# Kernel tuning notes

Hardware: AMD Instinct MI355X
Metric: run time of the kernel (lower is better)

Reference implementation:

```python
import jax, jax.numpy as jnp
import numpy as np

K_GRAD = 20        # num_nbrs for gradient operator
K_NORMAL = 10      # knn for normal/basis estimation
GRAD_REG = 1e-3    # grad_reg (lambda)
KERNEL_WIDTH = 1.0 # grad_kernel_width
EPS = 1e-8
N1, N2 = 8192, 8192
CHANNELS = [3, 64, 128, 256]


def knn_idx(pos, k):
    # brute-force kNN incl. self (loop=True, target_to_source)
    sq = jnp.sum(pos * pos, axis=1)
    d2 = sq[:, None] + sq[None, :] - 2.0 * (pos @ pos.T)
    _, idx = jax.lax.top_k(-d2, k)
    return idx  # [N, k]


def estimate_basis(pos, nbr, orientation):
    rel = pos[nbr] - pos[:, None, :]              # [N,k,3]
    cov = jnp.einsum('nki,nkj->nij', rel, rel)    # [N,3,3] local PCA
    _, vecs = jnp.linalg.eigh(cov)                # ascending eigenvalues
    normal, x_basis = vecs[:, :, 0], vecs[:, :, 2]
    sign = jnp.where(jnp.sum(normal * orientation, -1, keepdims=True) < 0.0, -1.0, 1.0)
    normal = normal * sign                        # orient along `orientation`
    y_basis = jnp.cross(normal, x_basis)
    return normal, x_basis, y_basis


def build_grad_div(pos, x_basis, y_basis, nbr):
    # regularized, Gaussian-weighted least-squares fit of a linear function per neighborhood
    rel = pos[nbr] - pos[:, None, :]              # [N,k,3]
    u = jnp.einsum('nkd,nd->nk', rel, x_basis)    # tangent coords
    v = jnp.einsum('nkd,nd->nk', rel, y_basis)
    dist = jnp.sqrt(jnp.sum(rel * rel, -1) + EPS)
    h = jnp.mean(dist, axis=1, keepdims=True)     # per-point bandwidth
    w = jnp.exp(-(dist * dist) / ((KERNEL_WIDTH * h) ** 2 + EPS))
    B = jnp.stack([jnp.ones_like(u), u, v], -1)   # [N,k,3] design matrix
    BtW = jnp.swapaxes(B, 1, 2) * w[:, None, :]   # [N,3,k]
    A = BtW @ B + GRAD_REG * jnp.eye(3, dtype=pos.dtype)
    C = jnp.linalg.solve(A, BtW)                  # [N,3,k] LS coefficients
    Gx, Gy = C[:, 1, :], C[:, 2, :]               # gradient stencils
    basis = jnp.stack([x_basis, y_basis], -1)     # [N,3,2]
    R = jnp.einsum('nda,nkdb->nkab', basis, basis[nbr])  # transport j->i, [N,k,2,2]
    return Gx, Gy, R


def grad_apply(Gx, Gy, nbr, f):
    fn = f[nbr]                                   # [N,k,C]
    return jnp.stack([jnp.einsum('nk,nkc->nc', Gx, fn),
                      jnp.einsum('nk,nkc->nc', Gy, fn)], 1)  # [N,2,C]


def div_apply(Gx, Gy, R, nbr, v):
    vt = jnp.einsum('nkab,nkbc->nkac', R, v[nbr])  # transported neighbor vectors
    return (jnp.einsum('nk,nkc->nc', Gx, vt[:, :, 0]) +
            jnp.einsum('nk,nkc->nc', Gy, vt[:, :, 1]))


def delta_conv(x, v, nbr, Gx, Gy, R, Ws, bs, Wv, bv, centralized):
    xn = x[nbr]
    if centralized:
        xn = xn - x[:, None, :]
    xmax = jnp.max(xn, axis=1)                    # max aggregation
    dv = div_apply(Gx, Gy, R, nbr, v)             # divergence
    Jv = jnp.stack([-v[:, 1], v[:, 0]], 1)        # 90-degree rotation
    cv = div_apply(Gx, Gy, R, nbr, Jv)            # curl = div(J v)
    x_out = jax.nn.relu(jnp.concatenate([xmax, dv, cv], -1) @ Ws + bs)
    if Wv is None:
        return x_out, v                            # last layer: scalar only
    gv = grad_apply(Gx, Gy, nbr, x_out)           # [N,2,Cout]
    vo = jnp.concatenate([v, gv], -1) @ Wv        # channel mix, no bias (equivariant)
    n = jnp.sqrt(jnp.sum(vo * vo, axis=1, keepdims=True) + EPS)
    vo = vo * (jax.nn.relu(n + bv) / (n + EPS))   # norm-gated vector nonlinearity
    return x_out, vo


def _forward(points, als_ppoints, params):
    pos = jnp.concatenate([points, als_ppoints], axis=0)  # [N,3]
    nbr = knn_idx(pos, K_GRAD)
    nbr_n = knn_idx(pos, K_NORMAL)
    _, xb, yb = estimate_basis(pos, nbr_n, orientation=pos)
    Gx, Gy, R = build_grad_div(pos, xb, yb, nbr)
    x = pos
    v = grad_apply(Gx, Gy, nbr, x)                # v = grad @ x
    out = []
    for i, (Ws, bs, Wv, bv) in enumerate(params):
        x, v = delta_conv(x, v, nbr, Gx, Gy, R, Ws, bs, Wv, bv, centralized=(i == 0))
        out.append(x)
    return tuple(out)


def setup_inputs():
    key = jax.random.key(0)
    ks = jax.random.split(key, 8)
    inp = {
        'points': jax.random.normal(ks[0], (N1, 3), jnp.float32),
        'als_ppoints': jax.random.normal(ks[1], (N2, 3), jnp.float32),
    }
    ki = 2
    for i in range(3):
        cin, cout = CHANNELS[i], CHANNELS[i + 1]
        inp[f'Ws{i}'] = jax.random.normal(ks[ki], (3 * cin, cout), jnp.float32) / np.sqrt(3.0 * cin)
        inp[f'bs{i}'] = jnp.zeros((cout,), jnp.float32)
        ki += 1
        if i < 2:
            inp[f'Wv{i}'] = jax.random.normal(ks[ki], (cin + cout, cout), jnp.float32) / np.sqrt(float(cin + cout))
            inp[f'bv{i}'] = jnp.zeros((cout,), jnp.float32)
            ki += 1
    return inp


def reference(points, als_ppoints, Ws0, bs0, Wv0, bv0, Ws1, bs1, Wv1, bv1, Ws2, bs2):
    params = [(Ws0, bs0, Wv0, bv0), (Ws1, bs1, Wv1, bv1), (Ws2, bs2, None, None)]
    return _forward(points, als_ppoints, params)
```

## Files before the change

### kernel.cpp

```cpp
#include <hip/hip_runtime.h>
#include <math.h>

#define NPTS 16384
#define KG 20
#define KN 10
#define KC 8
#define EPSF 1e-8f

#define GDIM 32
#define GL 4.75f
#define CW 0.296875f
#define GINV 3.3684210526f
#define RMAX 6

typedef __attribute__((ext_vector_type(8))) short short8v;
typedef __attribute__((ext_vector_type(4))) float floatx4;

__device__ __forceinline__ unsigned short f2bf(float v) {
  union { float f; unsigned u; } x;
  x.f = v;
  unsigned r = x.u + 0x7FFFu + ((x.u >> 16) & 1u);
  return (unsigned short)(r >> 16);
}

__device__ __forceinline__ float bf2f(unsigned short u) {
  union { unsigned u32; float f; } x;
  x.u32 = (unsigned)u << 16;
  return x.f;
}

#define KNN_INSERT(d2v, iv)                                                 \
  if ((d2v) < dist[KG - 1]) {                                               \
    dist[KG - 1] = (d2v); idx[KG - 1] = (iv);                               \
    _Pragma("unroll")                                                       \
    for (int s_ = KG - 1; s_ > 0; --s_) {                                   \
      if (dist[s_] < dist[s_ - 1]) {                                        \
        float td_ = dist[s_]; dist[s_] = dist[s_ - 1]; dist[s_ - 1] = td_;  \
        int ti_ = idx[s_]; idx[s_] = idx[s_ - 1]; idx[s_ - 1] = ti_;        \
      }                                                                     \
    }                                                                       \
  }

#define KNN_INSERT8(d2v, iv)                                                \
  if ((d2v) < dist[KC - 1]) {                                               \
    dist[KC - 1] = (d2v); idx[KC - 1] = (iv);                               \
    _Pragma("unroll")                                                       \
    for (int s_ = KC - 1; s_ > 0; --s_) {                                   \
      if (dist[s_] < dist[s_ - 1]) {                                        \
        float td_ = dist[s_]; dist[s_] = dist[s_ - 1]; dist[s_ - 1] = td_;  \
        int ti_ = idx[s_]; idx[s_] = idx[s_ - 1]; idx[s_ - 1] = ti_;        \
      }                                                                     \
    }                                                                       \
  }

__global__ __launch_bounds__(256) void posbin_kernel(const float* __restrict__ pts,
                                                     const float* __restrict__ als,
                                                     float4* __restrict__ pos4,
                                                     int* __restrict__ cell_count,
                                                     int* __restrict__ pt_cell) {
  int n = blockIdx.x * 256 + threadIdx.x;
  if (n >= NPTS) return;
  const float* src = (n < 8192) ? (pts + (size_t)n * 3) : (als + (size_t)(n - 8192) * 3);
  float x = src[0], y = src[1], z = src[2];
  pos4[n] = make_float4(x, y, z, 0.f);
  int cxi = (int)floorf((x + GL) * GINV); cxi = min(max(cxi, 0), GDIM - 1);
  int cyi = (int)floorf((y + GL) * GINV); cyi = min(max(cyi, 0), GDIM - 1);
  int czi = (int)floorf((z + GL) * GINV); czi = min(max(czi, 0), GDIM - 1);
  int c = (czi * GDIM + cyi) * GDIM + cxi;
  pt_cell[n] = c;
  atomicAdd(&cell_count[c], 1);
}

__global__ __launch_bounds__(256) void zero_kernel(int* __restrict__ cell_count,
                                                   int* __restrict__ fb_count) {
  int i = blockIdx.x * 256 + threadIdx.x;
  if (i < GDIM * GDIM * GDIM) cell_count[i] = 0;
  if (i == 0) *fb_count = 0;
}

__device__ __forceinline__ int cell_of(float x) {
  int c = (int)floorf((x + GL) * GINV);
  return min(max(c, 0), GDIM - 1);
}

__global__ __launch_bounds__(1024) void scan_kernel(const int* __restrict__ cell_count,
                                                    int* __restrict__ cell_start,
                                                    int* __restrict__ cell_cursor) {
  __shared__ int s[1024];
  int tid = threadIdx.x;
  int base = tid * 32;
  int local[32];
  int sum = 0;
#pragma unroll
  for (int i = 0; i < 32; ++i) { local[i] = cell_count[base + i]; sum += local[i]; }
  s[tid] = sum;
  __syncthreads();
  for (int off = 1; off < 1024; off <<= 1) {
    int v = (tid >= off) ? s[tid - off] : 0;
    __syncthreads();
    s[tid] += v;
    __syncthreads();
  }
  int run = s[tid] - sum;
#pragma unroll
  for (int i = 0; i < 32; ++i) {
    cell_start[base + i] = run;
    cell_cursor[base + i] = run;
    run += local[i];
  }
}

__global__ __launch_bounds__(256) void scatter_kernel(const float4* __restrict__ pos4,
                                                      const int* __restrict__ pt_cell,
                                                      int* __restrict__ cell_cursor,
                                                      float4* __restrict__ sorted4) {
  int i = blockIdx.x * 256 + threadIdx.x;
  if (i >= NPTS) return;
  int c = pt_cell[i];
  int dst = atomicAdd(&cell_cursor[c], 1);
  float4 p = pos4[i];
  p.w = __int_as_float(i);
  sorted4[dst] = p;
}

__global__ __launch_bounds__(256) void knn_grid_kernel(const float4* __restrict__ sorted4,
                                                       const int* __restrict__ cell_start,
                                                       const int* __restrict__ cell_count,
                                                       int* __restrict__ nbr,
                                                       int* __restrict__ fb_list,
                                                       int* __restrict__ fb_count) {
  int lane = threadIdx.x & 63;
  int sub = lane >> 5;
  int sl = lane & 31;
  int qs = blockIdx.x * 8 + (threadIdx.x >> 6) * 2 + sub;
  if (qs >= NPTS) return;
  float4 p = sorted4[qs];
  int q = __float_as_int(p.w);
  int cx = cell_of(p.x), cy = cell_of(p.y), cz = cell_of(p.z);
  float dist[KC];
  int idx[KC];
#pragma unroll
  for (int i = 0; i < KC; ++i) { dist[i] = 3.4e38f; idx[i] = 0; }

  {
    int tot = 0;
    int x0 = max(cx - 1, 0), x1 = min(cx + 1, GDIM - 1);
    int zlo = max(cz - 1, 0), zhi = min(cz + 1, GDIM - 1);
    int ylo = max(cy - 1, 0), yhi = min(cy + 1, GDIM - 1);
    for (int z = zlo; z <= zhi; ++z) {
      for (int y = ylo; y <= yhi; ++y) {
        int c0 = (z * GDIM + y) * GDIM + x0;
        int c1 = (z * GDIM + y) * GDIM + x1;
        int beg = cell_start[c0];
        int end = cell_start[c1] + cell_count[c1];
        int off = (sl - tot) & 31;
        for (int j = beg + off; j < end; j += 32) {
          float4 sp = sorted4[j];
          float dx = sp.x - p.x, dy = sp.y - p.y, dz = sp.z - p.z;
          float d2 = dx * dx + dy * dy + dz * dz;
          KNN_INSERT8(d2, __float_as_int(sp.w));
        }
        tot += end - beg;
      }
    }
  }
  int done;
  {
    float b2 = CW * CW;
    int cnt = 0;
#pragma unroll
    for (int i = 0; i < KC; ++i) cnt += (dist[i] <= b2) ? 1 : 0;
#pragma unroll
    for (int s = 1; s < 32; s <<= 1) cnt += __shfl_xor(cnt, s, 64);
    done = (cnt >= KG) ? 1 : 0;
  }

  for (int r = 2; r <= RMAX && !done; ++r) {
    int side = 2 * r + 1;
    int nt = side * side;
    for (int t = sl; t < nt; t += 32) {
      int dz = t / side - r;
      int dy = t - (dz + r) * side - r;
      int z = cz + dz, y = cy + dy;
      if (z < 0 || z >= GDIM || y < 0 || y >= GDIM) continue;
      int rowbase = (z * GDIM + y) * GDIM;
      if (dz == -r || dz == r || dy == -r || dy == r) {
        int xa = max(cx - r, 0), xb = min(cx + r, GDIM - 1);
        int beg = cell_start[rowbase + xa];
        int end = cell_start[rowbase + xb] + cell_count[rowbase + xb];
        for (int j = beg; j < end; ++j) {
          float4 sp = sorted4[j];
          float ddx = sp.x - p.x, ddy = sp.y - p.y, ddz = sp.z - p.z;
          float d2 = ddx * ddx + ddy * ddy + ddz * ddz;
          KNN_INSERT8(d2, __float_as_int(sp.w));
        }
      } else {
        int x = cx - r;
        if (x >= 0) {
          int c = rowbase + x;
          int beg = cell_start[c], end = beg + cell_count[c];
          for (int j = beg; j < end; ++j) {
            float4 sp = sorted4[j];
            float ddx = sp.x - p.x, ddy = sp.y - p.y, ddz = sp.z - p.z;
            float d2 = ddx * ddx + ddy * ddy + ddz * ddz;
            KNN_INSERT8(d2, __float_as_int(sp.w));
          }
        }
        x = cx + r;
        if (x < GDIM) {
          int c = rowbase + x;
          int beg = cell_start[c], end = beg + cell_count[c];
          for (int j = beg; j < end; ++j) {
            float4 sp = sorted4[j];
            float ddx = sp.x - p.x, ddy = sp.y - p.y, ddz = sp.z - p.z;
            float d2 = ddx * ddx + ddy * ddy + ddz * ddz;
            KNN_INSERT8(d2, __float_as_int(sp.w));
          }
        }
      }
    }
    float b = CW * (float)r;
    float b2 = b * b;
    int cnt = 0;
#pragma unroll
    for (int i = 0; i < KC; ++i) cnt += (dist[i] <= b2) ? 1 : 0;
#pragma unroll
    for (int s = 1; s < 32; s <<= 1) cnt += __shfl_xor(cnt, s, 64);
    if (cnt >= KG) done = 1;
  }

  int popc = 0, ovf = 0;
  for (int round = 0; round < KG; ++round) {
    unsigned long long key = ((unsigned long long)__float_as_uint(dist[0]) << 14) |
                             (unsigned long long)(unsigned)idx[0];
    unsigned long long m = key;
#pragma unroll
    for (int s = 1; s < 32; s <<= 1) {
      unsigned long long o = __shfl_xor(m, s, 64);
      if (o < m) m = o;
    }
    if (key == m) {
      nbr[(size_t)q * KG + round] = (int)(m & 0x3FFF);
#pragma unroll
      for (int s = 0; s < KC - 1; ++s) { dist[s] = dist[s + 1]; idx[s] = idx[s + 1]; }
      dist[KC - 1] = 3.4e38f;
      idx[KC - 1] = 0;
      if (++popc == KC) ovf = 1;
    }
  }
#pragma unroll
  for (int s = 1; s < 32; s <<= 1) ovf |= __shfl_xor(ovf, s, 64);
  if ((ovf || !done) && sl == 0) {
    int s = atomicAdd(fb_count, 1);
    fb_list[s] = qs;
  }
}

__global__ __launch_bounds__(256) void knn_fb_kernel(const float4* __restrict__ sorted4,
                                                     const int* __restrict__ fb_list,
                                                     const int* __restrict__ fb_count,
                                                     int* __restrict__ nbr) {
  __shared__ unsigned long long lists[256 * KG];
  __shared__ unsigned long long heads[256];
  __shared__ unsigned long long winner;
  int tid = threadIdx.x;
  int cnt = *fb_count;
  for (int qi = blockIdx.x; qi < cnt; qi += gridDim.x) {
    int t = fb_list[qi];
    float4 p = sorted4[t];
    int q = __float_as_int(p.w);
    float dist[KG];
    int idx[KG];
#pragma unroll
    for (int i = 0; i < KG; ++i) { dist[i] = 3.4e38f; idx[i] = 0; }
    int j0 = tid * 64;
    for (int j = j0; j < j0 + 64; ++j) {
      float4 c = sorted4[j];
      float dx = c.x - p.x, dy = c.y - p.y, dz = c.z - p.z;
      float d2 = dx * dx + dy * dy + dz * dz;
      KNN_INSERT(d2, __float_as_int(c.w));
    }
#pragma unroll
    for (int i = 0; i < KG; ++i)
      lists[tid * KG + i] = ((unsigned long long)__float_as_uint(dist[i]) << 22) |
                            ((unsigned long long)(unsigned)idx[i] << 8) |
                            (unsigned long long)tid;
    int hp = 0;
    __syncthreads();
    for (int round = 0; round < KG; ++round) {
      heads[tid] = (hp < KG) ? lists[tid * KG + hp] : ~0ull;
      __syncthreads();
      if (tid < 64) {
        unsigned long long m = heads[tid];
        unsigned long long o = heads[tid + 64];  if (o < m) m = o;
        o = heads[tid + 128]; if (o < m) m = o;
        o = heads[tid + 192]; if (o < m) m = o;
#pragma unroll
        for (int s = 32; s > 0; s >>= 1) {
          unsigned long long x = __shfl_xor(m, s, 64);
          if (x < m) m = x;
        }
        if (tid == 0) winner = m;
      }
      __syncthreads();
      unsigned long long w = winner;
      if (tid == (int)(w & 0xFF)) hp++;
      if (tid == 0) nbr[(size_t)q * KG + round] = (int)((w >> 8) & 0x3FFF);
      __syncthreads();
    }
  }
}

__global__ __launch_bounds__(256) void basis_kernel(const float4* __restrict__ pos4,
                                                    const int* __restrict__ nbr,
                                                    float4* __restrict__ xb4,
                                                    float4* __restrict__ yb4) {
  int n = blockIdx.x * 256 + threadIdx.x;
  if (n >= NPTS) return;
  float4 p = pos4[n];
  double c00 = 0, c01 = 0, c02 = 0, c11 = 0, c12 = 0, c22 = 0;
  for (int k = 0; k < KN; ++k) {
    int m = nbr[(size_t)n * KG + k];
    float4 pm = pos4[m];
    double dx = (double)pm.x - p.x, dy = (double)pm.y - p.y, dz = (double)pm.z - p.z;
    c00 += dx * dx; c01 += dx * dy; c02 += dx * dz;
    c11 += dy * dy; c12 += dy * dz; c22 += dz * dz;
  }
  double nx = 0, ny = 0, nz = 1;
  double p1 = c01 * c01 + c02 * c02 + c12 * c12;
  double qm = (c00 + c11 + c22) / 3.0;
  double g0 = c00 - qm, g1 = c11 - qm, g2 = c22 - qm;
  double p2 = g0 * g0 + g1 * g1 + g2 * g2 + 2.0 * p1;
  if (p2 > 1e-26) {
    double pp = sqrt(p2 / 6.0);
    double inv = 1.0 / pp;
    double b00 = g0 * inv, b11 = g1 * inv, b22 = g2 * inv;
    double b01 = c01 * inv, b02 = c02 * inv, b12 = c12 * inv;
    double detB = b00 * (b11 * b22 - b12 * b12) - b01 * (b01 * b22 - b12 * b02) +
                  b02 * (b01 * b12 - b11 * b02);
    double r = 0.5 * detB;
    r = fmin(1.0, fmax(-1.0, r));
    double phi = acos(r) / 3.0;
    double e1 = qm + 2.0 * pp * cos(phi);
    double e3 = qm + 2.0 * pp * cos(phi + 2.0943951023931953);
    double e2 = 3.0 * qm - e1 - e3;
    double a00 = c00 - e1, a11 = c11 - e1, a22 = c22 - e1;
    double f00 = c00 - e2, f11 = c11 - e2, f22 = c22 - e2;
    double u0 = a00 * f00 + c01 * c01 + c02 * c02;
    double u1 = c01 * f00 + a11 * c01 + c12 * c02;
    double u2 = c02 * f00 + c12 * c01 + a22 * c02;
    double v0 = a00 * c01 + c01 * f11 + c02 * c12;
    double v1 = c01 * c01 + a11 * f11 + c12 * c12;
    double v2 = c02 * c01 + c12 * f11 + a22 * c12;
    double w0 = a00 * c02 + c01 * c12 + c02 * f22;
    double w1 = c01 * c02 + a11 * c12 + c12 * f22;
    double w2 = c02 * c02 + c12 * c12 + a22 * f22;
    double nu = u0 * u0 + u1 * u1 + u2 * u2;
    double nv = v0 * v0 + v1 * v1 + v2 * v2;
    double nw = w0 * w0 + w1 * w1 + w2 * w2;
    double bx = u0, by = u1, bz = u2, bn = nu;
    if (nv > bn) { bx = v0; by = v1; bz = v2; bn = nv; }
    if (nw > bn) { bx = w0; by = w1; bz = w2; bn = nw; }
    if (bn > 1e-40) {
      double s = 1.0 / sqrt(bn);
      nx = bx * s; ny = by * s; nz = bz * s;
    }
  }
  double dotp = nx * p.x + ny * p.y + nz * p.z;
  if (dotp < 0.0) { nx = -nx; ny = -ny; nz = -nz; }
  double ax = fabs(nx), ay = fabs(ny), az = fabs(nz);
  double ex = 0, ey = 0, ez = 0;
  if (ax <= ay && ax <= az) ex = 1;
  else if (ay <= az) ey = 1;
  else ez = 1;
  double tx = ny * ez - nz * ey, ty = nz * ex - nx * ez, tz = nx * ey - ny * ex;
  double tn = 1.0 / sqrt(tx * tx + ty * ty + tz * tz);
  tx *= tn; ty *= tn; tz *= tn;
  double ux = ny * tz - nz * ty, uy = nz * tx - nx * tz, uz = nx * ty - ny * tx;
  xb4[n] = make_float4((float)tx, (float)ty, (float)tz, 0.f);
  yb4[n] = make_float4((float)ux, (float)uy, (float)uz, 0.f);
}

__global__ __launch_bounds__(256) void graddiv_kernel(const float4* __restrict__ pos4,
                                                      const int* __restrict__ nbr,
                                                      const float4* __restrict__ xb4,
                                                      const float4* __restrict__ yb4,
                                                      float* __restrict__ Gx,
                                                      float* __restrict__ Gy,
                                                      float2* __restrict__ C2,
                                                      float* __restrict__ v0) {
  int n = blockIdx.x * 256 + threadIdx.x;
  if (n >= NPTS) return;
  float4 p = pos4[n], xb = xb4[n], yb = yb4[n];
  float u[KG], vv[KG], w[KG];
  int mm[KG];
  float hsum = 0.f;
#pragma unroll
  for (int k = 0; k < KG; ++k) {
    int m = nbr[(size_t)n * KG + k];
    mm[k] = m;
    float4 pm = pos4[m];
    float rx = pm.x - p.x, ry = pm.y - p.y, rz = pm.z - p.z;
    u[k] = rx * xb.x + ry * xb.y + rz * xb.z;
    vv[k] = rx * yb.x + ry * yb.y + rz * yb.z;
    float dd = sqrtf(rx * rx + ry * ry + rz * rz + EPSF);
    w[k] = dd; hsum += dd;
  }
  float h = hsum * (1.f / KG);
  float invden = 1.f / (h * h + EPSF);
  double A00 = 0, A01 = 0, A02 = 0, A11 = 0, A12 = 0, A22 = 0;
#pragma unroll
  for (int k = 0; k < KG; ++k) {
    float wk = expf(-(w[k] * w[k]) * invden);
    w[k] = wk;
    A00 += wk; A01 += (double)wk * u[k]; A02 += (double)wk * vv[k];
    A11 += (double)wk * u[k] * u[k]; A12 += (double)wk * u[k] * vv[k];
    A22 += (double)wk * vv[k] * vv[k];
  }
  A00 += 0.001; A11 += 0.001; A22 += 0.001;
  double det = A00 * (A11 * A22 - A12 * A12) - A01 * (A01 * A22 - A12 * A02) +
               A02 * (A01 * A12 - A11 * A02);
  double idet = 1.0 / det;
  float i10 = (float)((A02 * A12 - A01 * A22) * idet);
  float i11 = (float)((A00 * A22 - A02 * A02) * idet);
  float i12 = (float)((A01 * A02 - A00 * A12) * idet);
  float i20 = (float)((A01 * A12 - A02 * A11) * idet);
  float i21 = i12;
  float i22 = (float)((A00 * A11 - A01 * A01) * idet);
  float a0x = 0, a0y = 0, a0z = 0, a1x = 0, a1y = 0, a1z = 0;
#pragma unroll
  for (int k = 0; k < KG; ++k) {
    float gx = w[k] * (i10 + i11 * u[k] + i12 * vv[k]);
    float gy = w[k] * (i20 + i21 * u[k] + i22 * vv[k]);
    Gx[(size_t)n * KG + k] = gx;
    Gy[(size_t)n * KG + k] = gy;
    int m = mm[k];
    float4 pm = pos4[m];
    a0x += gx * pm.x; a0y += gx * pm.y; a0z += gx * pm.z;
    a1x += gy * pm.x; a1y += gy * pm.y; a1z += gy * pm.z;
    float4 xm = xb4[m], ym = yb4[m];
    float g3x = gx * xb.x + gy * yb.x;
    float g3y = gx * xb.y + gy * yb.y;
    float g3z = gx * xb.z + gy * yb.z;
    float ca = g3x * xm.x + g3y * xm.y + g3z * xm.z;
    float cb = g3x * ym.x + g3y * ym.y + g3z * ym.z;
    C2[(size_t)n * KG + k] = make_float2(ca, cb);
  }
  v0[((size_t)n * 2 + 0) * 3 + 0] = a0x;
  v0[((size_t)n * 2 + 0) * 3 + 1] = a0y;
  v0[((size_t)n * 2 + 0) * 3 + 2] = a0z;
  v0[((size_t)n * 2 + 1) * 3 + 0] = a1x;
  v0[((size_t)n * 2 + 1) * 3 + 1] = a1y;
  v0[((size_t)n * 2 + 1) * 3 + 2] = a1z;
}

template <int CENTRAL>
__global__ __launch_bounds__(256) void feat16_kernel(const float* __restrict__ x, int ldx,
                                                     int cin,
                                                     const float* __restrict__ v,
                                                     const int* __restrict__ nbr,
                                                     const float2* __restrict__ C2,
                                                     unsigned short* __restrict__ feat, int Kp) {
  int per = Kp - 2 * cin;
  int gid = blockIdx.x * 256 + threadIdx.x;
  if (gid >= NPTS * per) return;
  int n = gid / per;
  int c = gid - n * per;
  size_t fb = (size_t)n * Kp;
  if (c >= cin) {
    feat[fb + 3 * cin + (c - cin)] = 0;
    return;
  }
  float xc = x[(size_t)n * ldx + c];
  float xmax = -3.4e38f, dv = 0.f, cv = 0.f;
  for (int k = 0; k < KG; ++k) {
    int m = nbr[(size_t)n * KG + k];
    float2 cc = C2[(size_t)n * KG + k];
    float xm = x[(size_t)m * ldx + c];
    xmax = fmaxf(xmax, CENTRAL ? (xm - xc) : xm);
    float va = v[((size_t)m * 2 + 0) * cin + c];
    float vb = v[((size_t)m * 2 + 1) * cin + c];
    dv += cc.x * va + cc.y * vb;
    cv += cc.y * va - cc.x * vb;
  }
  feat[fb + c] = f2bf(xmax);
  feat[fb + cin + c] = f2bf(dv);
  feat[fb + 2 * cin + c] = f2bf(cv);
}

__global__ __launch_bounds__(256) void feat16v8_kernel(const unsigned short* __restrict__ x,
                                                       int cin,
                                                       const unsigned short* __restrict__ v,
                                                       const int* __restrict__ nbr,
                                                       const float2* __restrict__ C2,
                                                       unsigned short* __restrict__ feat) {
  int per = cin >> 3;
  int gid = blockIdx.x * 256 + threadIdx.x;
  if (gid >= NPTS * per) return;
  int n = gid / per;
  int c8 = (gid - n * per) << 3;
  float xmax[8], dv[8], cv[8];
#pragma unroll
  for (int i = 0; i < 8; ++i) { xmax[i] = -3.4e38f; dv[i] = 0.f; cv[i] = 0.f; }
  const int* nrow = nbr + (size_t)n * KG;
  const float2* crow = C2 + (size_t)n * KG;
#pragma unroll 4
  for (int k = 0; k < KG; ++k) {
    int m = nrow[k];
    float2 cc = crow[k];
    short8v xm = *reinterpret_cast<const short8v*>(x + (size_t)m * cin + c8);
    short8v va = *reinterpret_cast<const short8v*>(v + ((size_t)m * 2 + 0) * cin + c8);
    short8v vb = *reinterpret_cast<const short8v*>(v + ((size_t)m * 2 + 1) * cin + c8);
#pragma unroll
    for (int i = 0; i < 8; ++i) {
      float xf = bf2f((unsigned short)xm[i]);
      float af = bf2f((unsigned short)va[i]);
      float bf = bf2f((unsigned short)vb[i]);
      xmax[i] = fmaxf(xmax[i], xf);
      dv[i] += cc.x * af + cc.y * bf;
      cv[i] += cc.y * af - cc.x * bf;
    }
  }
  size_t fb = (size_t)n * (3 * cin);
  short8v o0, o1, o2;
#pragma unroll
  for (int i = 0; i < 8; ++i) {
    o0[i] = (short)f2bf(xmax[i]);
    o1[i] = (short)f2bf(dv[i]);
    o2[i] = (short)f2bf(cv[i]);
  }
  *reinterpret_cast<short8v*>(&feat[fb + c8]) = o0;
  *reinterpret_cast<short8v*>(&feat[fb + cin + c8]) = o1;
  *reinterpret_cast<short8v*>(&feat[fb + 2 * cin + c8]) = o2;
}

__global__ __launch_bounds__(256) void vin16_kernel(const float* __restrict__ v, int cin,
                                                    const unsigned short* __restrict__ xout,
                                                    int cout,
                                                    const int* __restrict__ nbr,
                                                    const float* __restrict__ Gx,
                                                    const float* __restrict__ Gy,
                                                    unsigned short* __restrict__ vinb, int Kp,
                                                    int total) {
  int gid = blockIdx.x * 256 + threadIdx.x;
  if (gid >= total) return;
  int n = gid / Kp;
  int c = gid - n * Kp;
  int K = cin + cout;
  unsigned short o0, o1;
  if (c < cin) {
    o0 = f2bf(v[((size_t)n * 2 + 0) * cin + c]);
    o1 = f2bf(v[((size_t)n * 2 + 1) * cin + c]);
  } else if (c < K) {
    int cc = c - cin;
    float a0 = 0.f, a1 = 0.f;
    for (int k = 0; k < KG; ++k) {
      int m = nbr[(size_t)n * KG + k];
      float f = bf2f(xout[(size_t)m * cout + cc]);
      a0 += Gx[(size_t)n * KG + k] * f;
      a1 += Gy[(size_t)n * KG + k] * f;
    }
    o0 = f2bf(a0);
    o1 = f2bf(a1);
  } else {
    o0 = 0; o1 = 0;
  }
  vinb[((size_t)n * 2 + 0) * Kp + c] = o0;
  vinb[((size_t)n * 2 + 1) * Kp + c] = o1;
}

__global__ __launch_bounds__(256) void vin16v8_kernel(const unsigned short* __restrict__ v,
                                                      int cin,
                                                      const unsigned short* __restrict__ xout,
                                                      int cout,
                                                      const int* __restrict__ nbr,
                                                      const float* __restrict__ Gx,
                                                      const float* __restrict__ Gy,
                                                      unsigned short* __restrict__ vinb,
                                                      int Kp) {
  int per = Kp >> 3;
  int gid = blockIdx.x * 256 + threadIdx.x;
  if (gid >= NPTS * per) return;
  int n = gid / per;
  int c8 = (gid - n * per) << 3;
  short8v o0, o1;
  if (c8 < cin) {
    o0 = *reinterpret_cast<const short8v*>(v + ((size_t)n * 2 + 0) * cin + c8);
    o1 = *reinterpret_cast<const short8v*>(v + ((size_t)n * 2 + 1) * cin + c8);
  } else {
    int cc8 = c8 - cin;
    float a0[8], a1[8];
#pragma unroll
    for (int i = 0; i < 8; ++i) { a0[i] = 0.f; a1[i] = 0.f; }
    const int* nrow = nbr + (size_t)n * KG;
    const float* gxr = Gx + (size_t)n * KG;
    const float* gyr = Gy + (size_t)n * KG;
#pragma unroll 4
    for (int k = 0; k < KG; ++k) {
      int m = nrow[k];
      float gx = gxr[k], gy = gyr[k];
      short8v f = *reinterpret_cast<const short8v*>(xout + (size_t)m * cout + cc8);
#pragma unroll
      for (int i = 0; i < 8; ++i) {
        float ff = bf2f((unsigned short)f[i]);
        a0[i] += gx * ff;
        a1[i] += gy * ff;
      }
    }
#pragma unroll
    for (int i = 0; i < 8; ++i) {
      o0[i] = (short)f2bf(a0[i]);
      o1[i] = (short)f2bf(a1[i]);
    }
  }
  *reinterpret_cast<short8v*>(&vinb[((size_t)n * 2 + 0) * Kp + c8]) = o0;
  *reinterpret_cast<short8v*>(&vinb[((size_t)n * 2 + 1) * Kp + c8]) = o1;
}

__device__ __forceinline__ void wprep_one(const float* W, unsigned short* Wt, int K, int Kp,
                                          int N, int i) {
  int n = i / Kp, k = i - n * Kp;
  Wt[i] = (k < K) ? f2bf(W[(size_t)k * N + n]) : (unsigned short)0;
}

__global__ __launch_bounds__(256) void wprep_all_kernel(const float* __restrict__ Ws0,
                                                        const float* __restrict__ Wv0,
                                                        const float* __restrict__ Ws1,
                                                        const float* __restrict__ Wv1,
                                                        const float* __restrict__ Ws2,
                                                        unsigned short* __restrict__ Wt_s0,
                                                        unsigned short* __restrict__ Wt_v0,
                                                        unsigned short* __restrict__ Wt_s1,
                                                        unsigned short* __restrict__ Wt_v1,
                                                        unsigned short* __restrict__ Wt_s2) {
  int gid = blockIdx.x * 256 + threadIdx.x;
  if (gid < 2048) wprep_one(Ws0, Wt_s0, 9, 32, 64, gid);
  else if (gid < 8192) wprep_one(Wv0, Wt_v0, 67, 96, 64, gid - 2048);
  else if (gid < 32768) wprep_one(Ws1, Wt_s1, 192, 192, 128, gid - 8192);
  else if (gid < 57344) wprep_one(Wv1, Wt_v1, 192, 192, 128, gid - 32768);
  else if (gid < 155648) wprep_one(Ws2, Wt_s2, 384, 384, 256, gid - 57344);
}

template <int MODE>
__global__ __launch_bounds__(256) void gemm16_kernel(const unsigned short* __restrict__ A,
                                                     const unsigned short* __restrict__ Bt,
                                                     const float* __restrict__ bias,
                                                     float* __restrict__ Cf,
                                                     unsigned short* __restrict__ Cb,
                                                     int Kp, int Ncol) {
  int lane = threadIdx.x & 63;
  int wave = threadIdx.x >> 6;
  int rowBase = blockIdx.y * 64 + wave * 16;
  int colBase = blockIdx.x * 64;
  int lr = lane & 15;
  int kg = (lane >> 4) * 8;
  floatx4 acc0 = {0.f, 0.f, 0.f, 0.f};
  floatx4 acc1 = acc0, acc2 = acc0, acc3 = acc0;
  const unsigned short* arow = A + (size_t)(rowBase + lr) * Kp + kg;
  const unsigned short* b0p = Bt + (size_t)(colBase + lr) * Kp + kg;
  for (int k0 = 0; k0 < Kp; k0 += 32) {
    short8v a = *reinterpret_cast<const short8v*>(arow + k0);
    short8v b0 = *reinterpret_cast<const short8v*>(b0p + k0);
    short8v b1 = *reinterpret_cast<const short8v*>(b0p + (size_t)16 * Kp + k0);
    short8v b2 = *reinterpret_cast<const short8v*>(b0p + (size_t)32 * Kp + k0);
    short8v b3 = *reinterpret_cast<const short8v*>(b0p + (size_t)48 * Kp + k0);
    acc0 = __builtin_amdgcn_mfma_f32_16x16x32_bf16(a, b0, acc0, 0, 0, 0);
    acc1 = __builtin_amdgcn_mfma_f32_16x16x32_bf16(a, b1, acc1, 0, 0, 0);
    acc2 = __builtin_amdgcn_mfma_f32_16x16x32_bf16(a, b2, acc2, 0, 0, 0);
    acc3 = __builtin_amdgcn_mfma_f32_16x16x32_bf16(a, b3, acc3, 0, 0, 0);
  }
  int rsub = (lane >> 4) * 4;
  floatx4 accs[4] = {acc0, acc1, acc2, acc3};
#pragma unroll
  for (int nb = 0; nb < 4; ++nb) {
    int col = colBase + nb * 16 + lr;
    float bb = bias[col];
    if (MODE == 0) {
#pragma unroll
      for (int r = 0; r < 4; ++r) {
        int row = rowBase + rsub + r;
        float val = fmaxf(accs[nb][r] + bb, 0.f);
        Cf[(size_t)row * Ncol + col] = val;
        if (Cb) Cb[(size_t)row * Ncol + col] = f2bf(val);
      }
    } else {
#pragma unroll
      for (int pr = 0; pr < 2; ++pr) {
        float a0 = accs[nb][2 * pr], a1 = accs[nb][2 * pr + 1];
        float nrm = sqrtf(a0 * a0 + a1 * a1 + EPSF);
        float s = fmaxf(nrm + bb, 0.f) / (nrm + EPSF);
        int row = rowBase + rsub + 2 * pr;
        Cb[(size_t)row * Ncol + col] = f2bf(a0 * s);
        Cb[(size_t)(row + 1) * Ncol + col] = f2bf(a1 * s);
      }
    }
  }
}

extern "C" void kernel_launch(void* const* d_in, const int* in_sizes, int n_in,
                              void* d_out, int out_size, void* d_ws, size_t ws_size,
                              hipStream_t stream) {
  const float* pts = (const float*)d_in[0];
  const float* als = (const float*)d_in[1];
  const float* Ws0 = (const float*)d_in[2];
  const float* bs0 = (const float*)d_in[3];
  const float* Wv0 = (const float*)d_in[4];
  const float* bv0 = (const float*)d_in[5];
  const float* Ws1 = (const float*)d_in[6];
  const float* bs1 = (const float*)d_in[7];
  const float* Wv1 = (const float*)d_in[8];
  const float* bv1 = (const float*)d_in[9];
  const float* Ws2 = (const float*)d_in[10];
  const float* bs2 = (const float*)d_in[11];

  char* ws = (char*)d_ws;
  float4* pos4 = (float4*)(ws + 0);
  int* nbr = (int*)(ws + 262144);
  float4* xb4 = (float4*)(ws + 1572864);
  float4* yb4 = (float4*)(ws + 1835008);
  float* Gx = (float*)(ws + 2097152);
  float* Gy = (float*)(ws + 3407872);
  float2* C2 = (float2*)(ws + 4718592);
  float* v0f = (float*)(ws + 7340032);
  unsigned short* vb_a = (unsigned short*)(ws + 8388608);
  unsigned short* vb_b = (unsigned short*)(ws + 17825792);
  unsigned short* xb0m = (unsigned short*)(ws + 23068672);
  unsigned short* xb1m = (unsigned short*)(ws + 26214400);
  unsigned short* stg = (unsigned short*)(ws + 31457280);
  char* wtb = ws + 45088768;
  unsigned short* Wt_s0 = (unsigned short*)(wtb + 0);
  unsigned short* Wt_v0 = (unsigned short*)(wtb + 4096);
  unsigned short* Wt_s1 = (unsigned short*)(wtb + 16384);
  unsigned short* Wt_v1 = (unsigned short*)(wtb + 65536);
  unsigned short* Wt_s2 = (unsigned short*)(wtb + 114688);

  char* gws = ws + 46137344;
  int* cell_count = (int*)(gws + 0);
  int* cell_start = (int*)(gws + 131072);
  int* cell_cursor = (int*)(gws + 262144);
  int* pt_cell = (int*)(gws + 393216);
  int* fb_list = (int*)(gws + 458752);
  int* fb_count = (int*)(gws + 524288);
  float4* sorted4 = (float4*)(gws + 528384);

  float* out0 = (float*)d_out;
  float* out1 = out0 + (size_t)NPTS * 64;
  float* out2 = out1 + (size_t)NPTS * 128;

  zero_kernel<<<(GDIM * GDIM * GDIM + 255) / 256, 256, 0, stream>>>(cell_count, fb_count);
  posbin_kernel<<<64, 256, 0, stream>>>(pts, als, pos4, cell_count, pt_cell);
  scan_kernel<<<1, 1024, 0, stream>>>(cell_count, cell_start, cell_cursor);
  scatter_kernel<<<64, 256, 0, stream>>>(pos4, pt_cell, cell_cursor, sorted4);
  knn_grid_kernel<<<NPTS / 8, 256, 0, stream>>>(sorted4, cell_start, cell_count, nbr, fb_list,
                                                fb_count);
  knn_fb_kernel<<<128, 256, 0, stream>>>(sorted4, fb_list, fb_count, nbr);

  basis_kernel<<<64, 256, 0, stream>>>(pos4, nbr, xb4, yb4);
  graddiv_kernel<<<64, 256, 0, stream>>>(pos4, nbr, xb4, yb4, Gx, Gy, C2, v0f);

  wprep_all_kernel<<<608, 256, 0, stream>>>(Ws0, Wv0, Ws1, Wv1, Ws2, Wt_s0, Wt_v0, Wt_s1,
                                            Wt_v1, Wt_s2);

  feat16_kernel<1><<<(NPTS * 26 + 255) / 256, 256, 0, stream>>>((const float*)pos4, 4, 3, v0f,
                                                                nbr, C2, stg, 32);
  gemm16_kernel<0><<<dim3(1, 256), 256, 0, stream>>>(stg, Wt_s0, bs0, out0, xb0m, 32, 64);
  vin16_kernel<<<(NPTS * 96 + 255) / 256, 256, 0, stream>>>(v0f, 3, xb0m, 64, nbr, Gx, Gy, stg,
                                                            96, NPTS * 96);
  gemm16_kernel<1><<<dim3(1, 512), 256, 0, stream>>>(stg, Wt_v0, bv0, nullptr, vb_b, 96, 64);

  feat16v8_kernel<<<NPTS * 8 / 256, 256, 0, stream>>>(xb0m, 64, vb_b, nbr, C2, stg);
  gemm16_kernel<0><<<dim3(2, 256), 256, 0, stream>>>(stg, Wt_s1, bs1, out1, xb1m, 192, 128);
  vin16v8_kernel<<<NPTS * 24 / 256, 256, 0, stream>>>(vb_b, 64, xb1m, 128, nbr, Gx, Gy, stg,
                                                      192);
  gemm16_kernel<1><<<dim3(2, 512), 256, 0, stream>>>(stg, Wt_v1, bv1, nullptr, vb_a, 192, 128);

  feat16v8_kernel<<<NPTS * 16 / 256, 256, 0, stream>>>(xb1m, 128, vb_a, nbr, C2, stg);
  gemm16_kernel<0><<<dim3(4, 256), 256, 0, stream>>>(stg, Wt_s2, bs2, out2, nullptr, 384, 256);
}
```

Measured before the change: 322.1 us.

## Run whole pipeline in spatially sorted point order, unpermute only final outputs

Points are now indexed by their grid-sorted position throughout kNN, basis, grad/div and feature gathers, and a sortmap permutes rows back to original order only when the float outputs are written. Neighbour gathers then hit spatially local memory, which should improve cache hit rates in the gather-heavy feature and stencil kernels. The cost is an extra map array plus scattered row writes in the GEMM epilogue.

```diff
diff --git a/kernel.cpp b/kernel.cpp
--- a/kernel.cpp
+++ b/kernel.cpp
@@ -113,7 +113,8 @@
 __global__ __launch_bounds__(256) void scatter_kernel(const float4* __restrict__ pos4,
                                                       const int* __restrict__ pt_cell,
                                                       int* __restrict__ cell_cursor,
-                                                      float4* __restrict__ sorted4) {
+                                                      float4* __restrict__ sorted4,
+                                                      int* __restrict__ sortmap) {
   int i = blockIdx.x * 256 + threadIdx.x;
   if (i >= NPTS) return;
   int c = pt_cell[i];
@@ -121,6 +122,7 @@
   float4 p = pos4[i];
   p.w = __int_as_float(i);
   sorted4[dst] = p;
+  sortmap[dst] = i;
 }
 
 __global__ __launch_bounds__(256) void knn_grid_kernel(const float4* __restrict__ sorted4,
@@ -135,7 +137,6 @@
   int qs = blockIdx.x * 8 + (threadIdx.x >> 6) * 2 + sub;
   if (qs >= NPTS) return;
   float4 p = sorted4[qs];
-  int q = __float_as_int(p.w);
   int cx = cell_of(p.x), cy = cell_of(p.y), cz = cell_of(p.z);
   float dist[KC];
   int idx[KC];
@@ -158,7 +159,7 @@
           float4 sp = sorted4[j];
           float dx = sp.x - p.x, dy = sp.y - p.y, dz = sp.z - p.z;
           float d2 = dx * dx + dy * dy + dz * dz;
-          KNN_INSERT8(d2, __float_as_int(sp.w));
+          KNN_INSERT8(d2, j);
         }
         tot += end - beg;
       }
@@ -192,7 +193,7 @@
           float4 sp = sorted4[j];
           float ddx = sp.x - p.x, ddy = sp.y - p.y, ddz = sp.z - p.z;
           float d2 = ddx * ddx + ddy * ddy + ddz * ddz;
-          KNN_INSERT8(d2, __float_as_int(sp.w));
+          KNN_INSERT8(d2, j);
         }
       } else {
         int x = cx - r;
@@ -203,7 +204,7 @@
             float4 sp = sorted4[j];
             float ddx = sp.x - p.x, ddy = sp.y - p.y, ddz = sp.z - p.z;
             float d2 = ddx * ddx + ddy * ddy + ddz * ddz;
-            KNN_INSERT8(d2, __float_as_int(sp.w));
+            KNN_INSERT8(d2, j);
           }
         }
         x = cx + r;
@@ -214,7 +215,7 @@
             float4 sp = sorted4[j];
             float ddx = sp.x - p.x, ddy = sp.y - p.y, ddz = sp.z - p.z;
             float d2 = ddx * ddx + ddy * ddy + ddz * ddz;
-            KNN_INSERT8(d2, __float_as_int(sp.w));
+            KNN_INSERT8(d2, j);
           }
         }
       }
@@ -240,7 +241,7 @@
       if (o < m) m = o;
     }
     if (key == m) {
-      nbr[(size_t)q * KG + round] = (int)(m & 0x3FFF);
+      nbr[(size_t)qs * KG + round] = (int)(m & 0x3FFF);
 #pragma unroll
       for (int s = 0; s < KC - 1; ++s) { dist[s] = dist[s + 1]; idx[s] = idx[s + 1]; }
       dist[KC - 1] = 3.4e38f;
@@ -268,7 +269,6 @@
   for (int qi = blockIdx.x; qi < cnt; qi += gridDim.x) {
     int t = fb_list[qi];
     float4 p = sorted4[t];
-    int q = __float_as_int(p.w);
     float dist[KG];
     int idx[KG];
 #pragma unroll
@@ -278,7 +278,7 @@
       float4 c = sorted4[j];
       float dx = c.x - p.x, dy = c.y - p.y, dz = c.z - p.z;
       float d2 = dx * dx + dy * dy + dz * dz;
-      KNN_INSERT(d2, __float_as_int(c.w));
+      KNN_INSERT(d2, j);
     }
 #pragma unroll
     for (int i = 0; i < KG; ++i)
@@ -305,23 +305,23 @@
       __syncthreads();
       unsigned long long w = winner;
       if (tid == (int)(w & 0xFF)) hp++;
-      if (tid == 0) nbr[(size_t)q * KG + round] = (int)((w >> 8) & 0x3FFF);
+      if (tid == 0) nbr[(size_t)t * KG + round] = (int)((w >> 8) & 0x3FFF);
       __syncthreads();
     }
   }
 }
 
-__global__ __launch_bounds__(256) void basis_kernel(const float4* __restrict__ pos4,
+__global__ __launch_bounds__(256) void basis_kernel(const float4* __restrict__ sorted4,
                                                     const int* __restrict__ nbr,
                                                     float4* __restrict__ xb4,
                                                     float4* __restrict__ yb4) {
   int n = blockIdx.x * 256 + threadIdx.x;
   if (n >= NPTS) return;
-  float4 p = pos4[n];
+  float4 p = sorted4[n];
   double c00 = 0, c01 = 0, c02 = 0, c11 = 0, c12 = 0, c22 = 0;
   for (int k = 0; k < KN; ++k) {
     int m = nbr[(size_t)n * KG + k];
-    float4 pm = pos4[m];
+    float4 pm = sorted4[m];
     double dx = (double)pm.x - p.x, dy = (double)pm.y - p.y, dz = (double)pm.z - p.z;
     c00 += dx * dx; c01 += dx * dy; c02 += dx * dz;
     c11 += dy * dy; c12 += dy * dz; c22 += dz * dz;
@@ -381,7 +381,7 @@
   yb4[n] = make_float4((float)ux, (float)uy, (float)uz, 0.f);
 }
 
-__global__ __launch_bounds__(256) void graddiv_kernel(const float4* __restrict__ pos4,
+__global__ __launch_bounds__(256) void graddiv_kernel(const float4* __restrict__ sorted4,
                                                       const int* __restrict__ nbr,
                                                       const float4* __restrict__ xb4,
                                                       const float4* __restrict__ yb4,
@@ -391,7 +391,7 @@
                                                       float* __restrict__ v0) {
   int n = blockIdx.x * 256 + threadIdx.x;
   if (n >= NPTS) return;
-  float4 p = pos4[n], xb = xb4[n], yb = yb4[n];
+  float4 p = sorted4[n], xb = xb4[n], yb = yb4[n];
   float u[KG], vv[KG], w[KG];
   int mm[KG];
   float hsum = 0.f;
@@ -399,7 +399,7 @@
   for (int k = 0; k < KG; ++k) {
     int m = nbr[(size_t)n * KG + k];
     mm[k] = m;
-    float4 pm = pos4[m];
+    float4 pm = sorted4[m];
     float rx = pm.x - p.x, ry = pm.y - p.y, rz = pm.z - p.z;
     u[k] = rx * xb.x + ry * xb.y + rz * xb.z;
     vv[k] = rx * yb.x + ry * yb.y + rz * yb.z;
@@ -435,7 +435,7 @@
     Gx[(size_t)n * KG + k] = gx;
     Gy[(size_t)n * KG + k] = gy;
     int m = mm[k];
-    float4 pm = pos4[m];
+    float4 pm = sorted4[m];
     a0x += gx * pm.x; a0y += gx * pm.y; a0z += gx * pm.z;
     a1x += gy * pm.x; a1y += gy * pm.y; a1z += gy * pm.z;
     float4 xm = xb4[m], ym = yb4[m];
@@ -647,6 +647,7 @@
                                                      const float* __restrict__ bias,
                                                      float* __restrict__ Cf,
                                                      unsigned short* __restrict__ Cb,
+                                                     const int* __restrict__ rowmap,
                                                      int Kp, int Ncol) {
   int lane = threadIdx.x & 63;
   int wave = threadIdx.x >> 6;
@@ -671,6 +672,11 @@
   }
   int rsub = (lane >> 4) * 4;
   floatx4 accs[4] = {acc0, acc1, acc2, acc3};
+  int orow[4];
+  if (MODE == 0) {
+#pragma unroll
+    for (int r = 0; r < 4; ++r) orow[r] = rowmap[rowBase + rsub + r];
+  }
 #pragma unroll
   for (int nb = 0; nb < 4; ++nb) {
     int col = colBase + nb * 16 + lr;
@@ -680,7 +686,7 @@
       for (int r = 0; r < 4; ++r) {
         int row = rowBase + rsub + r;
         float val = fmaxf(accs[nb][r] + bb, 0.f);
-        Cf[(size_t)row * Ncol + col] = val;
+        Cf[(size_t)orow[r] * Ncol + col] = val;
         if (Cb) Cb[(size_t)row * Ncol + col] = f2bf(val);
       }
     } else {
@@ -742,6 +748,7 @@
   int* fb_list = (int*)(gws + 458752);
   int* fb_count = (int*)(gws + 524288);
   float4* sorted4 = (float4*)(gws + 528384);
+  int* sortmap = (int*)(gws + 790528);
 
   float* out0 = (float*)d_out;
   float* out1 = out0 + (size_t)NPTS * 64;
@@ -750,30 +757,35 @@
   zero_kernel<<<(GDIM * GDIM * GDIM + 255) / 256, 256, 0, stream>>>(cell_count, fb_count);
   posbin_kernel<<<64, 256, 0, stream>>>(pts, als, pos4, cell_count, pt_cell);
   scan_kernel<<<1, 1024, 0, stream>>>(cell_count, cell_start, cell_cursor);
-  scatter_kernel<<<64, 256, 0, stream>>>(pos4, pt_cell, cell_cursor, sorted4);
+  scatter_kernel<<<64, 256, 0, stream>>>(pos4, pt_cell, cell_cursor, sorted4, sortmap);
   knn_grid_kernel<<<NPTS / 8, 256, 0, stream>>>(sorted4, cell_start, cell_count, nbr, fb_list,
                                                 fb_count);
   knn_fb_kernel<<<128, 256, 0, stream>>>(sorted4, fb_list, fb_count, nbr);
 
-  basis_kernel<<<64, 256, 0, stream>>>(pos4, nbr, xb4, yb4);
-  graddiv_kernel<<<64, 256, 0, stream>>>(pos4, nbr, xb4, yb4, Gx, Gy, C2, v0f);
+  basis_kernel<<<64, 256, 0, stream>>>(sorted4, nbr, xb4, yb4);
+  graddiv_kernel<<<64, 256, 0, stream>>>(sorted4, nbr, xb4, yb4, Gx, Gy, C2, v0f);
 
   wprep_all_kernel<<<608, 256, 0, stream>>>(Ws0, Wv0, Ws1, Wv1, Ws2, Wt_s0, Wt_v0, Wt_s1,
                                             Wt_v1, Wt_s2);
 
-  feat16_kernel<1><<<(NPTS * 26 + 255) / 256, 256, 0, stream>>>((const float*)pos4, 4, 3, v0f,
-                                                                nbr, C2, stg, 32);
-  gemm16_kernel<0><<<dim3(1, 256), 256, 0, stream>>>(stg, Wt_s0, bs0, out0, xb0m, 32, 64);
+  feat16_kernel<1><<<(NPTS * 26 + 255) / 256, 256, 0, stream>>>((const float*)sorted4, 4, 3,
+                                                                v0f, nbr, C2, stg, 32);
+  gemm16_kernel<0><<<dim3(1, 256), 256, 0, stream>>>(stg, Wt_s0, bs0, out0, xb0m, sortmap, 32,
+                                                     64);
   vin16_kernel<<<(NPTS * 96 + 255) / 256, 256, 0, stream>>>(v0f, 3, xb0m, 64, nbr, Gx, Gy, stg,
                                                             96, NPTS * 96);
-  gemm16_kernel<1><<<dim3(1, 512), 256, 0, stream>>>(stg, Wt_v0, bv0, nullptr, vb_b, 96, 64);
+  gemm16_kernel<1><<<dim3(1, 512), 256, 0, stream>>>(stg, Wt_v0, bv0, nullptr, vb_b, nullptr,
+                                                     96, 64);
 
   feat16v8_kernel<<<NPTS * 8 / 256, 256, 0, stream>>>(xb0m, 64, vb_b, nbr, C2, stg);
-  gemm16_kernel<0><<<dim3(2, 256), 256, 0, stream>>>(stg, Wt_s1, bs1, out1, xb1m, 192, 128);
+  gemm16_kernel<0><<<dim3(2, 256), 256, 0, stream>>>(stg, Wt_s1, bs1, out1, xb1m, sortmap, 192,
+                                                     128);
   vin16v8_kernel<<<NPTS * 24 / 256, 256, 0, stream>>>(vb_b, 64, xb1m, 128, nbr, Gx, Gy, stg,
                                                       192);
-  gemm16_kernel<1><<<dim3(2, 512), 256, 0, stream>>>(stg, Wt_v1, bv1, nullptr, vb_a, 192, 128);
+  gemm16_kernel<1><<<dim3(2, 512), 256, 0, stream>>>(stg, Wt_v1, bv1, nullptr, vb_a, nullptr,
+                                                     192, 128);
 
   feat16v8_kernel<<<NPTS * 16 / 256, 256, 0, stream>>>(xb1m, 128, vb_a, nbr, C2, stg);
-  gemm16_kernel<0><<<dim3(4, 256), 256, 0, stream>>>(stg, Wt_s2, bs2, out2, nullptr, 384, 256);
-}
+  gemm16_kernel<0><<<dim3(4, 256), 256, 0, stream>>>(stg, Wt_s2, bs2, out2, nullptr, sortmap,
+                                                     384, 256);
+}
```

Result: faster. 299.1 us (-7.1%).
